# Optimization experiments

Hardware: AMD Instinct MI355X
Metric: run time of the kernel (lower is better)

The kernel has to match this reference:

```python
import jax, jax.numpy as jnp
import numpy as np

N, C, OUT, E, H = 4096, 256, 256, 131072, 8
DH = C // H
EPS = 1e-5


def layer_norm(h, g, b):
    mu = jnp.mean(h, axis=-1, keepdims=True)
    var = jnp.mean(jnp.square(h - mu), axis=-1, keepdims=True)
    return (h - mu) * jax.lax.rsqrt(var + EPS) * g + b


def setup_inputs() -> dict:
    key = jax.random.key(0)
    ks = jax.random.split(key, 12)
    s = 1.0 / np.sqrt(C)
    return {
        "x": jax.random.normal(ks[0], (N, C), jnp.float32),
        "edge_index": jax.random.randint(ks[1], (2, E), 0, N, jnp.int32),
        "edge_attr": jax.random.normal(ks[2], (E, C), jnp.float32),
        # nn.MultiheadAttention params
        "in_proj_w": jax.random.uniform(ks[3], (3 * C, C), jnp.float32, -s, s),
        "in_proj_b": jnp.zeros((3 * C,), jnp.float32),
        "attn_out_w": jax.random.uniform(ks[4], (C, C), jnp.float32, -s, s),
        "attn_out_b": jnp.zeros((C,), jnp.float32),
        # edge_mlp: Linear(3C -> OUT) + LayerNorm(OUT)
        "edge_w": jax.random.uniform(ks[5], (OUT, 3 * C), jnp.float32, -1 / np.sqrt(3 * C), 1 / np.sqrt(3 * C)),
        "edge_b": jax.random.uniform(ks[6], (OUT,), jnp.float32, -1 / np.sqrt(3 * C), 1 / np.sqrt(3 * C)),
        "ln1_g": jnp.ones((OUT,), jnp.float32),
        "ln1_b": jnp.zeros((OUT,), jnp.float32),
        # output_proj: Linear(C + OUT -> OUT)
        "out_w": jax.random.uniform(ks[7], (OUT, C + OUT), jnp.float32, -1 / np.sqrt(C + OUT), 1 / np.sqrt(C + OUT)),
        "out_b": jax.random.uniform(ks[8], (OUT,), jnp.float32, -1 / np.sqrt(C + OUT), 1 / np.sqrt(C + OUT)),
        "ln2_g": jnp.ones((OUT,), jnp.float32),
        "ln2_b": jnp.zeros((OUT,), jnp.float32),
    }


def reference(x, edge_index, edge_attr, in_proj_w, in_proj_b, attn_out_w, attn_out_b,
              edge_w, edge_b, ln1_g, ln1_b, out_w, out_b, ln2_g, ln2_b):
    num_nodes = x.shape[0]
    # --- dense self-attention over all nodes (seq len = N, batch 1) ---
    qkv = x @ in_proj_w.T + in_proj_b            # [N, 3C]
    q, k, v = jnp.split(qkv, 3, axis=-1)
    q = q.reshape(num_nodes, H, DH).transpose(1, 0, 2)  # [H, N, DH]
    k = k.reshape(num_nodes, H, DH).transpose(1, 0, 2)
    v = v.reshape(num_nodes, H, DH).transpose(1, 0, 2)
    scores = jnp.einsum("hqd,hkd->hqk", q, k) / np.sqrt(DH)
    attn = jax.nn.softmax(scores, axis=-1)       # dropout inactive at eval
    ctx = jnp.einsum("hqk,hkd->hqd", attn, v)    # [H, N, DH]
    ctx = ctx.transpose(1, 0, 2).reshape(num_nodes, C)
    x_attn = ctx @ attn_out_w.T + attn_out_b     # [N, C]
    # --- vectorized edge messages: gather -> MLP -> scatter-add ---
    row, col = edge_index[0], edge_index[1]
    msg_in = jnp.concatenate([x[row], x[col], edge_attr], axis=-1)  # [E, 3C]
    msg = jax.nn.relu(layer_norm(msg_in @ edge_w.T + edge_b, ln1_g, ln1_b))
    node_messages = jax.ops.segment_sum(msg, col, num_segments=num_nodes)  # [N, OUT]
    # --- combine, project, residual, norm ---
    combined = jnp.concatenate([x_attn, node_messages], axis=-1)
    out = combined @ out_w.T + out_b
    out = out + x                                # OUT == C so residual fires
    return layer_norm(out, ln2_g, ln2_b)
```

## Files before the change

### kernel.cpp

```cpp
#include <hip/hip_runtime.h>
#include <hip/hip_bf16.h>
#include <math.h>

typedef __bf16 bf16;
typedef __bf16 bf16x8 __attribute__((ext_vector_type(8)));
typedef __bf16 bf16x4 __attribute__((ext_vector_type(4)));
typedef float f32x4 __attribute__((ext_vector_type(4)));
typedef float f32x16 __attribute__((ext_vector_type(16)));

#define MFMA16(a, b, c) __builtin_amdgcn_mfma_f32_16x16x32_bf16((a), (b), (c), 0, 0, 0)
#define MFMA32(a, b, c) __builtin_amdgcn_mfma_f32_32x32x16_bf16((a), (b), (c), 0, 0, 0)

#define N_NODES 4096
#define C_DIM   256
#define E_EDGES 131072

__device__ __forceinline__ float ldf(const void* p, int i, bool f32) {
    return f32 ? ((const float*)p)[i] : (float)((const bf16*)p)[i];
}

__device__ __forceinline__ bf16x8 ld8(const void* base, size_t off, bool f32) {
    if (f32) {
        const float* p = (const float*)base + off;
        float4 a = *(const float4*)p;
        float4 b = *(const float4*)(p + 4);
        bf16x8 r;
        r[0] = (bf16)a.x; r[1] = (bf16)a.y; r[2] = (bf16)a.z; r[3] = (bf16)a.w;
        r[4] = (bf16)b.x; r[5] = (bf16)b.y; r[6] = (bf16)b.z; r[7] = (bf16)b.w;
        return r;
    }
    return *(const bf16x8*)((const bf16*)base + off);
}

__device__ __forceinline__ unsigned cvtpk(float a, float b) {
    unsigned r;
    asm("v_cvt_pk_bf16_f32 %0, %1, %2" : "=v"(r) : "v"(a), "v"(b));
    return r;
}
__device__ __forceinline__ void pl32swap(unsigned &a, unsigned &b) {
    asm volatile("v_permlane32_swap_b32 %0, %1" : "+v"(a), "+v"(b));
}

union PW { unsigned u[4]; bf16x8 v; };

__global__ __launch_bounds__(64) void detect_dtype(const void* x, int* flag)
{
    const bf16* xb = (const bf16*)x;
    int tid = threadIdx.x;
    int bad = 0;
    for (int i = tid; i < 4096; i += 64) {
        float v = fabsf((float)xb[i]);
        if (!(v >= 1e-6f && v <= 100.0f)) bad++;
    }
#pragma unroll
    for (int m = 1; m < 64; m <<= 1) bad += __shfl_xor(bad, m);
    if (tid == 0) *flag = (bad > 400) ? 1 : 0;
}

__global__ __launch_bounds__(256) void convert_inputs(
    const void* s0, const void* s1, const void* s2, const void* s3, const void* s4,
    bf16* dst, const int* flag)
{
    int idx = blockIdx.x * 256 + threadIdx.x;
    const void* src; int local;
    if (idx < 1048576)      { src = s0; local = idx; }
    else if (idx < 1245184) { src = s1; local = idx - 1048576; }
    else if (idx < 1310720) { src = s2; local = idx - 1245184; }
    else if (idx < 1507328) { src = s3; local = idx - 1310720; }
    else                    { src = s4; local = idx - 1507328; }
    if (*flag) dst[idx] = (bf16)(((const float*)src)[local]);
    else ((unsigned short*)dst)[idx] = ((const unsigned short*)src)[local];
}

__global__ __launch_bounds__(256) void edge_hist(
    const int* __restrict__ ecol, int* __restrict__ counts)
{
    int e = blockIdx.x * 256 + threadIdx.x;
    atomicAdd(&counts[ecol[e]], 1);
}

__global__ __launch_bounds__(256) void edge_scan(
    const int* __restrict__ counts, int* __restrict__ offsets,
    int* __restrict__ cursor)
{
    __shared__ int part[256];
    __shared__ int pref[257];
    int t = threadIdx.x;
    int base = t * 16;
    int s = 0;
#pragma unroll
    for (int i = 0; i < 16; ++i) s += counts[base + i];
    part[t] = s;
    __syncthreads();
    if (t == 0) {
        int run = 0;
        for (int i = 0; i < 256; ++i) { pref[i] = run; run += part[i]; }
        pref[256] = run;
    }
    __syncthreads();
    int off = pref[t];
#pragma unroll
    for (int i = 0; i < 16; ++i) {
        offsets[base + i] = off;
        cursor[base + i]  = off;
        off += counts[base + i];
    }
    if (t == 255) offsets[4096] = off;
}

__global__ __launch_bounds__(256) void edge_scatter(
    const int* __restrict__ ecol, int* __restrict__ cursor,
    int* __restrict__ eid)
{
    int e = blockIdx.x * 256 + threadIdx.x;
    int pos = atomicAdd(&cursor[ecol[e]], 1);
    eid[pos] = e;
}

__global__ __launch_bounds__(256) void gemm_bt(
    const bf16* __restrict__ A, int lda,
    const bf16* __restrict__ W, int ldw,
    const void* __restrict__ bias,
    void* __restrict__ Cout, int ldc, int c_f32,
    const bf16* __restrict__ resid, int ldr,
    int K, const int* __restrict__ flag)
{
    const bool f32 = (*flag != 0);
    const int wave = threadIdx.x >> 6;
    const int lane = threadIdx.x & 63;
    const int quad = lane >> 4;
    const int l16  = lane & 15;
    const int m_base = blockIdx.x * 32;
    const int n_base = blockIdx.y * 256 + wave * 64;

    const bf16* a0p = A + (size_t)(m_base + l16) * lda + quad * 8;
    const bf16* a1p = a0p + (size_t)16 * lda;
    const bf16* wp  = W + (size_t)(n_base + l16) * ldw + quad * 8;

    f32x4 acc[2][4] = {};
    for (int k = 0; k < K; k += 32) {
        bf16x8 a0 = *(const bf16x8*)(a0p + k);
        bf16x8 a1 = *(const bf16x8*)(a1p + k);
#pragma unroll
        for (int nt = 0; nt < 4; ++nt) {
            bf16x8 b = *(const bf16x8*)(wp + (size_t)nt * 16 * ldw + k);
            acc[0][nt] = MFMA16(a0, b, acc[0][nt]);
            acc[1][nt] = MFMA16(a1, b, acc[1][nt]);
        }
    }
#pragma unroll
    for (int mt = 0; mt < 2; ++mt) {
#pragma unroll
        for (int nt = 0; nt < 4; ++nt) {
            int col = n_base + nt * 16 + l16;
            float bv = bias ? ldf(bias, col, f32) : 0.0f;
#pragma unroll
            for (int r = 0; r < 4; ++r) {
                int row = m_base + mt * 16 + quad * 4 + r;
                float v = acc[mt][nt][r] + bv;
                if (resid) v += (float)resid[(size_t)row * ldr + col];
                if (c_f32) ((float*)Cout)[(size_t)row * ldc + col] = v;
                else       ((bf16*)Cout)[(size_t)row * ldc + col] = (bf16)v;
            }
        }
    }
}

__global__ __launch_bounds__(256) void gemm_uv(
    const bf16* __restrict__ x, const bf16* __restrict__ ew,
    bf16* __restrict__ U, bf16* __restrict__ V)
{
    const int wave = threadIdx.x >> 6;
    const int lane = threadIdx.x & 63;
    const int quad = lane >> 4;
    const int l16  = lane & 15;
    const int m_base = blockIdx.x * 32;
    bf16* dst = blockIdx.y ? V : U;
    const bf16* W = ew + blockIdx.y * 256;

    const bf16* a0p = x + (size_t)(m_base + l16) * 256 + quad * 8;
    const bf16* a1p = a0p + (size_t)16 * 256;
    const bf16* wp  = W + (size_t)(wave * 64 + l16) * 768 + quad * 8;

    f32x4 acc[2][4] = {};
#pragma unroll
    for (int kk = 0; kk < 8; ++kk) {
        int k = kk * 32;
        bf16x8 a0 = *(const bf16x8*)(a0p + k);
        bf16x8 a1 = *(const bf16x8*)(a1p + k);
#pragma unroll
        for (int nt = 0; nt < 4; ++nt) {
            bf16x8 b = *(const bf16x8*)(wp + (size_t)nt * 16 * 768 + k);
            acc[0][nt] = MFMA16(a0, b, acc[0][nt]);
            acc[1][nt] = MFMA16(a1, b, acc[1][nt]);
        }
    }
#pragma unroll
    for (int mt = 0; mt < 2; ++mt)
#pragma unroll
        for (int nt = 0; nt < 4; ++nt) {
            int col = wave * 64 + nt * 16 + l16;
#pragma unroll
            for (int r = 0; r < 4; ++r) {
                int row = m_base + mt * 16 + quad * 4 + r;
                dst[(size_t)row * 256 + col] = (bf16)acc[mt][nt][r];
            }
        }
}

__global__ __launch_bounds__(256) void transpose_v(
    const bf16* __restrict__ qkv, bf16* __restrict__ vt)
{
    __shared__ bf16 t[32][65];
    const int n0 = blockIdx.x * 64;
    const int c0 = blockIdx.y * 32;
    const int tid = threadIdx.x;
    {
        int cl = tid & 31, nl = tid >> 5;
#pragma unroll
        for (int p = 0; p < 8; ++p) {
            int n = nl + p * 8;
            t[cl][n] = qkv[(size_t)(n0 + n) * 768 + 512 + c0 + cl];
        }
    }
    __syncthreads();
    {
        int nn = tid & 63, cc = tid >> 6;
#pragma unroll
        for (int p = 0; p < 8; ++p) {
            int c = cc + p * 4;
            vt[(size_t)(c0 + c) * 4096 + n0 + nn] = t[c][nn];
        }
    }
}

__global__ __launch_bounds__(256) void attn_kernel(
    const bf16* __restrict__ qkv,
    const bf16* __restrict__ vt,
    bf16* __restrict__ ctx)
{
    __shared__ float oL[4][32][33];
    __shared__ float mS[4][32];
    __shared__ float lS[4][32];
    const int tid  = threadIdx.x;
    const int wave = tid >> 6;
    const int lane = tid & 63;
    const int l32  = lane & 31;
    const int hl   = lane >> 5;
    const int h  = blockIdx.x >> 7;
    const int qt = blockIdx.x & 127;

    const float csc = 1.4426950408889634f * 0.17677669529663687f;

    const bf16* qrow = qkv + (size_t)(qt * 32 + l32) * 768 + h * 32 + hl * 8;
    bf16x8 qf1 = *(const bf16x8*)qrow;
    bf16x8 qf2 = *(const bf16x8*)(qrow + 16);

    const bf16* kbp = qkv + 256 + h * 32 + hl * 8;
    const bf16* vrp = vt + (size_t)(h * 32 + l32) * 4096 + hl * 8;

    float mrun = -INFINITY, msc = -INFINITY, lacc = 0.f;
    f32x16 oacc = {};
    const f32x16 z16 = {};

    const int kbeg = wave * 1024;
    for (int k0 = kbeg; k0 < kbeg + 1024; k0 += 32) {
        const bf16* kp = kbp + (size_t)(k0 + l32) * 768;
        bf16x8 kf1 = *(const bf16x8*)kp;
        bf16x8 kf2 = *(const bf16x8*)(kp + 16);
        bf16x8 vf1 = *(const bf16x8*)(vrp + k0);
        bf16x8 vf2 = *(const bf16x8*)(vrp + k0 + 16);

        f32x16 s = MFMA32(kf1, qf1, z16);
        s = MFMA32(kf2, qf2, s);

        float a0 = fmaxf(fmaxf(s[0], s[1]), fmaxf(s[2], s[3]));
        float a1 = fmaxf(fmaxf(s[4], s[5]), fmaxf(s[6], s[7]));
        float a2 = fmaxf(fmaxf(s[8], s[9]), fmaxf(s[10], s[11]));
        float a3 = fmaxf(fmaxf(s[12], s[13]), fmaxf(s[14], s[15]));
        float tm = fmaxf(fmaxf(a0, a1), fmaxf(a2, a3));
        tm = fmaxf(tm, __shfl_xor(tm, 32));

        if (__any(tm > mrun)) {
            float nm = fmaxf(mrun, tm);
            float nmsc = nm * csc;
            float al = exp2f(msc - nmsc);
            mrun = nm; msc = nmsc;
            lacc *= al;
#pragma unroll
            for (int i = 0; i < 16; ++i) oacc[i] *= al;
        }

        float p[16];
#pragma unroll
        for (int i = 0; i < 16; ++i) {
            p[i] = exp2f(__builtin_fmaf(s[i], csc, -msc));
            lacc += p[i];
        }

        unsigned w0 = cvtpk(p[0], p[1]),  w1 = cvtpk(p[2], p[3]);
        unsigned w2 = cvtpk(p[4], p[5]),  w3 = cvtpk(p[6], p[7]);
        unsigned w4 = cvtpk(p[8], p[9]),  w5 = cvtpk(p[10], p[11]);
        unsigned w6 = cvtpk(p[12], p[13]), w7 = cvtpk(p[14], p[15]);
        pl32swap(w0, w2); pl32swap(w1, w3);
        pl32swap(w4, w6); pl32swap(w5, w7);
        PW f1; f1.u[0] = w0; f1.u[1] = w1; f1.u[2] = w2; f1.u[3] = w3;
        PW f2; f2.u[0] = w4; f2.u[1] = w5; f2.u[2] = w6; f2.u[3] = w7;

        oacc = MFMA32(vf1, f1.v, oacc);
        oacc = MFMA32(vf2, f2.v, oacc);
    }

    lacc += __shfl_xor(lacc, 32);
    if (hl == 0) { mS[wave][l32] = mrun; lS[wave][l32] = lacc; }
#pragma unroll
    for (int i = 0; i < 16; ++i) {
        int d = (i & 3) + 8 * (i >> 2) + 4 * hl;
        oL[wave][l32][d] = oacc[i];
    }
    __syncthreads();
    {
        int q = tid >> 3, d0 = (tid & 7) * 4;
        float m0 = mS[0][q], m1 = mS[1][q], m2 = mS[2][q], m3 = mS[3][q];
        float ms = fmaxf(fmaxf(m0, m1), fmaxf(m2, m3));
        float f0 = exp2f((m0 - ms) * csc), f1 = exp2f((m1 - ms) * csc);
        float f2 = exp2f((m2 - ms) * csc), f3 = exp2f((m3 - ms) * csc);
        float ls = lS[0][q] * f0 + lS[1][q] * f1 + lS[2][q] * f2 + lS[3][q] * f3;
        float inv = 1.0f / ls;
        bf16x4 o4;
#pragma unroll
        for (int i = 0; i < 4; ++i) {
            int d = d0 + i;
            float v = (oL[0][q][d] * f0 + oL[1][q][d] * f1 +
                       oL[2][q][d] * f2 + oL[3][q][d] * f3) * inv;
            o4[i] = (bf16)v;
        }
        *(bf16x4*)(ctx + (size_t)(qt * 32 + q) * 256 + h * 32 + d0) = o4;
    }
}

__global__ __launch_bounds__(256, 4) void edge_msg_v5(
    const int* __restrict__ erow, const int* __restrict__ ecol,
    const void* __restrict__ eattr,
    const bf16* __restrict__ ew,
    const void* __restrict__ eb,
    const void* __restrict__ g1, const void* __restrict__ b1,
    const bf16* __restrict__ U, const bf16* __restrict__ V,
    bf16* __restrict__ msg, const int* __restrict__ flag)
{
    __shared__ float stats[32][4][2];
    const bool f32 = (*flag != 0);
    const int tid  = threadIdx.x;
    const int colq = tid >> 6;
    const int lane = tid & 63;
    const int quad = lane >> 4;
    const int l16  = lane & 15;
    const int e_base = blockIdx.x * 32;

    const bf16* wp = ew + (size_t)(colq * 64 + l16) * 768 + 512 + quad * 8;

    f32x4 acc[2][4] = {};
#pragma unroll
    for (int k0 = 0; k0 < 8; ++k0) {
        bf16x8 b[4];
#pragma unroll
        for (int nt = 0; nt < 4; ++nt)
            b[nt] = *(const bf16x8*)(wp + (size_t)nt * 16 * 768 + k0 * 32);
#pragma unroll
        for (int mt = 0; mt < 2; ++mt) {
            bf16x8 a = ld8(eattr,
                (size_t)(e_base + mt * 16 + l16) * 256 + k0 * 32 + quad * 8, f32);
#pragma unroll
            for (int nt = 0; nt < 4; ++nt)
                acc[mt][nt] = MFMA16(a, b[nt], acc[mt][nt]);
        }
    }

    float ebv[4], glv[4], blv[4];
#pragma unroll
    for (int nt = 0; nt < 4; ++nt) {
        int col = colq * 64 + nt * 16 + l16;
        ebv[nt] = ldf(eb, col, f32);
        glv[nt] = ldf(g1, col, f32);
        blv[nt] = ldf(b1, col, f32);
    }
    int erw[2][4], ecl[2][4];
#pragma unroll
    for (int mt = 0; mt < 2; ++mt)
#pragma unroll
        for (int r = 0; r < 4; ++r) {
            int e = e_base + mt * 16 + quad * 4 + r;
            erw[mt][r] = erow[e];
            ecl[mt][r] = ecol[e];
        }

    float s[2][4] = {}, q[2][4] = {};
#pragma unroll
    for (int mt = 0; mt < 2; ++mt)
#pragma unroll
        for (int nt = 0; nt < 4; ++nt) {
            int col = colq * 64 + nt * 16 + l16;
#pragma unroll
            for (int r = 0; r < 4; ++r) {
                float u = (float)U[(size_t)erw[mt][r] * 256 + col];
                float v = (float)V[(size_t)ecl[mt][r] * 256 + col];
                float val = acc[mt][nt][r] + ebv[nt] + u + v;
                acc[mt][nt][r] = val;
                s[mt][r] += val;
                q[mt][r] = __builtin_fmaf(val, val, q[mt][r]);
            }
        }
#pragma unroll
    for (int msk = 1; msk < 16; msk <<= 1)
#pragma unroll
        for (int mt = 0; mt < 2; ++mt)
#pragma unroll
            for (int r = 0; r < 4; ++r) {
                s[mt][r] += __shfl_xor(s[mt][r], msk);
                q[mt][r] += __shfl_xor(q[mt][r], msk);
            }
    if (l16 == 0) {
#pragma unroll
        for (int mt = 0; mt < 2; ++mt)
#pragma unroll
            for (int r = 0; r < 4; ++r) {
                int row = mt * 16 + quad * 4 + r;
                stats[row][colq][0] = s[mt][r];
                stats[row][colq][1] = q[mt][r];
            }
    }
    __syncthreads();
#pragma unroll
    for (int mt = 0; mt < 2; ++mt)
#pragma unroll
        for (int r = 0; r < 4; ++r) {
            int row = mt * 16 + quad * 4 + r;
            float ss = (stats[row][0][0] + stats[row][1][0]) +
                       (stats[row][2][0] + stats[row][3][0]);
            float qq = (stats[row][0][1] + stats[row][1][1]) +
                       (stats[row][2][1] + stats[row][3][1]);
            float mean = ss * (1.0f / 256.0f);
            float var  = qq * (1.0f / 256.0f) - mean * mean;
            float rstd = rsqrtf(var + 1e-5f);
            bf16* op = msg + (size_t)(e_base + row) * 256;
#pragma unroll
            for (int nt = 0; nt < 4; ++nt) {
                int col = colq * 64 + nt * 16 + l16;
                float o = fmaxf((acc[mt][nt][r] - mean) * rstd * glv[nt] + blv[nt], 0.0f);
                op[col] = (bf16)o;
            }
        }
}

__global__ __launch_bounds__(256) void node_gather(
    const bf16* __restrict__ msg,
    const int* __restrict__ offsets, const int* __restrict__ eid,
    bf16* __restrict__ combined)
{
    const int wave = threadIdx.x >> 6, lane = threadIdx.x & 63;
    const int node = blockIdx.x * 4 + wave;
    const int start = offsets[node];
    const int cnt   = offsets[node + 1] - start;
    float a0 = 0.f, a1 = 0.f, a2 = 0.f, a3 = 0.f;
    int i = 0;
    for (; i + 4 <= cnt; i += 4) {
        int e0 = eid[start + i],     e1 = eid[start + i + 1];
        int e2 = eid[start + i + 2], e3 = eid[start + i + 3];
        bf16x4 r0 = *(const bf16x4*)(msg + (size_t)e0 * 256 + lane * 4);
        bf16x4 r1 = *(const bf16x4*)(msg + (size_t)e1 * 256 + lane * 4);
        bf16x4 r2 = *(const bf16x4*)(msg + (size_t)e2 * 256 + lane * 4);
        bf16x4 r3 = *(const bf16x4*)(msg + (size_t)e3 * 256 + lane * 4);
        a0 += (float)r0[0] + (float)r1[0] + (float)r2[0] + (float)r3[0];
        a1 += (float)r0[1] + (float)r1[1] + (float)r2[1] + (float)r3[1];
        a2 += (float)r0[2] + (float)r1[2] + (float)r2[2] + (float)r3[2];
        a3 += (float)r0[3] + (float)r1[3] + (float)r2[3] + (float)r3[3];
    }
    for (; i < cnt; ++i) {
        int e = eid[start + i];
        bf16x4 r = *(const bf16x4*)(msg + (size_t)e * 256 + lane * 4);
        a0 += (float)r[0]; a1 += (float)r[1]; a2 += (float)r[2]; a3 += (float)r[3];
    }
    bf16* cp = combined + (size_t)node * 512 + 256 + lane * 4;
    cp[0] = (bf16)a0; cp[1] = (bf16)a1; cp[2] = (bf16)a2; cp[3] = (bf16)a3;
}

__global__ __launch_bounds__(256) void edge_node(
    const bf16* __restrict__ x,
    const int* __restrict__ erow,
    const void* __restrict__ eattr,
    const bf16* __restrict__ ew,
    const void* __restrict__ eb,
    const void* __restrict__ g1, const void* __restrict__ b1,
    const int* __restrict__ offsets, const int* __restrict__ eid,
    bf16* __restrict__ combined, const int* __restrict__ flag)
{
    __shared__ float part[32][4][2];
    const bool f32 = (*flag != 0);
    const int wave = threadIdx.x >> 6;
    const int lane = threadIdx.x & 63;
    const int quad = lane >> 4;
    const int l16  = lane & 15;
    const int n = blockIdx.x;
    const int start = offsets[n];
    const int cnt   = offsets[n + 1] - start;

    float gv[4], bv[4], ebv[4];
#pragma unroll
    for (int nt = 0; nt < 4; ++nt) {
        int col = wave * 64 + nt * 16 + l16;
        gv[nt]  = ldf(g1, col, f32);
        bv[nt]  = ldf(b1, col, f32);
        ebv[nt] = ldf(eb, col, f32);
    }
    const bf16* wp = ew + (size_t)(wave * 64 + l16) * 768 + quad * 8;
    const bf16* xn = x + (size_t)n * 256 + quad * 8;

    f32x4 acc1[4] = {};
#pragma unroll
    for (int kk = 0; kk < 8; ++kk) {
        bf16x8 a = *(const bf16x8*)(xn + kk * 32);
#pragma unroll
        for (int nt = 0; nt < 4; ++nt) {
            bf16x8 b = *(const bf16x8*)(wp + (size_t)nt * 16 * 768 + 256 + kk * 32);
            acc1[nt] = MFMA16(a, b, acc1[nt]);
        }
    }
    float nacc[4] = {0.f, 0.f, 0.f, 0.f};
    for (int c0 = 0; c0 < cnt; c0 += 32) {
        int i0 = c0 + l16;      i0 = (i0 < cnt) ? i0 : 0;
        int i1 = c0 + 16 + l16; i1 = (i1 < cnt) ? i1 : 0;
        int e0 = eid[start + i0];
        int e1 = eid[start + i1];
        const bf16* xr0 = x + (size_t)erow[e0] * 256 + quad * 8;
        const bf16* xr1 = x + (size_t)erow[e1] * 256 + quad * 8;
        f32x4 acc[2][4];
#pragma unroll
        for (int nt = 0; nt < 4; ++nt) { acc[0][nt] = acc1[nt]; acc[1][nt] = acc1[nt]; }
#pragma unroll
        for (int kk = 0; kk < 8; ++kk) {
            bf16x8 a0 = *(const bf16x8*)(xr0 + kk * 32);
            bf16x8 a1 = *(const bf16x8*)(xr1 + kk * 32);
#pragma unroll
            for (int nt = 0; nt < 4; ++nt) {
                bf16x8 b = *(const bf16x8*)(wp + (size_t)nt * 16 * 768 + kk * 32);
                acc[0][nt] = MFMA16(a0, b, acc[0][nt]);
                acc[1][nt] = MFMA16(a1, b, acc[1][nt]);
            }
        }
#pragma unroll
        for (int kk = 0; kk < 8; ++kk) {
            int koff = quad * 8 + kk * 32;
            bf16x8 a0 = ld8(eattr, (size_t)e0 * 256 + koff, f32);
            bf16x8 a1 = ld8(eattr, (size_t)e1 * 256 + koff, f32);
#pragma unroll
            for (int nt = 0; nt < 4; ++nt) {
                bf16x8 b = *(const bf16x8*)(wp + (size_t)nt * 16 * 768 + 512 + kk * 32);
                acc[0][nt] = MFMA16(a0, b, acc[0][nt]);
                acc[1][nt] = MFMA16(a1, b, acc[1][nt]);
            }
        }
#pragma unroll
        for (int mt = 0; mt < 2; ++mt)
#pragma unroll
            for (int nt = 0; nt < 4; ++nt)
#pragma unroll
                for (int r = 0; r < 4; ++r) acc[mt][nt][r] += ebv[nt];
        float ps[2][4], pq[2][4];
#pragma unroll
        for (int mt = 0; mt < 2; ++mt)
#pragma unroll
            for (int r = 0; r < 4; ++r) {
                float s = 0.f, q = 0.f;
#pragma unroll
                for (int nt = 0; nt < 4; ++nt) {
                    float v = acc[mt][nt][r];
                    s += v; q += v * v;
                }
                ps[mt][r] = s; pq[mt][r] = q;
            }
#pragma unroll
        for (int msk = 1; msk < 16; msk <<= 1)
#pragma unroll
            for (int mt = 0; mt < 2; ++mt)
#pragma unroll
                for (int r = 0; r < 4; ++r) {
                    ps[mt][r] += __shfl_xor(ps[mt][r], msk);
                    pq[mt][r] += __shfl_xor(pq[mt][r], msk);
                }
        if (l16 == 0) {
#pragma unroll
            for (int mt = 0; mt < 2; ++mt)
#pragma unroll
                for (int r = 0; r < 4; ++r) {
                    part[mt * 16 + quad * 4 + r][wave][0] = ps[mt][r];
                    part[mt * 16 + quad * 4 + r][wave][1] = pq[mt][r];
                }
        }
        __syncthreads();
#pragma unroll
        for (int mt = 0; mt < 2; ++mt)
#pragma unroll
            for (int r = 0; r < 4; ++r) {
                int row = mt * 16 + quad * 4 + r;
                float s = part[row][0][0] + part[row][1][0] + part[row][2][0] + part[row][3][0];
                float q = part[row][0][1] + part[row][1][1] + part[row][2][1] + part[row][3][1];
                float mean = s * (1.0f / 256.0f);
                float var  = q * (1.0f / 256.0f) - mean * mean;
                float rstd = rsqrtf(var + 1e-5f);
                if ((c0 + row) < cnt) {
#pragma unroll
                    for (int nt = 0; nt < 4; ++nt) {
                        float val = (acc[mt][nt][r] - mean) * rstd * gv[nt] + bv[nt];
                        nacc[nt] += fmaxf(val, 0.0f);
                    }
                }
            }
        __syncthreads();
    }
#pragma unroll
    for (int nt = 0; nt < 4; ++nt) {
        nacc[nt] += __shfl_xor(nacc[nt], 16);
        nacc[nt] += __shfl_xor(nacc[nt], 32);
    }
    if (quad == 0) {
#pragma unroll
        for (int nt = 0; nt < 4; ++nt)
            combined[(size_t)n * 512 + 256 + wave * 64 + nt * 16 + l16] = (bf16)nacc[nt];
    }
}

__global__ __launch_bounds__(256) void gemm_ln(
    const bf16* __restrict__ A,
    const bf16* __restrict__ W,
    const void* __restrict__ bias,
    const bf16* __restrict__ resid,
    const void* __restrict__ g, const void* __restrict__ bb,
    void* __restrict__ out, const int* __restrict__ flag)
{
    __shared__ float stats[16][4][2];
    const bool f32 = (*flag != 0);
    const int wave = threadIdx.x >> 6;
    const int lane = threadIdx.x & 63;
    const int quad = lane >> 4;
    const int l16  = lane & 15;
    const int m_base = blockIdx.x * 16;

    const bf16* ap = A + (size_t)(m_base + l16) * 512 + quad * 8;
    const bf16* wp = W + (size_t)(wave * 64 + l16) * 512 + quad * 8;

    f32x4 acc[4] = {};
#pragma unroll
    for (int kk = 0; kk < 16; ++kk) {
        int k = kk * 32;
        bf16x8 a = *(const bf16x8*)(ap + k);
#pragma unroll
        for (int nt = 0; nt < 4; ++nt) {
            bf16x8 b = *(const bf16x8*)(wp + (size_t)nt * 16 * 512 + k);
            acc[nt] = MFMA16(a, b, acc[nt]);
        }
    }
    float s[4] = {}, q[4] = {};
#pragma unroll
    for (int nt = 0; nt < 4; ++nt) {
        int col = wave * 64 + nt * 16 + l16;
        float bv = ldf(bias, col, f32);
#pragma unroll
        for (int r = 0; r < 4; ++r) {
            int row = m_base + quad * 4 + r;
            float v = acc[nt][r] + bv + (float)resid[(size_t)row * 256 + col];
            acc[nt][r] = v;
            s[r] += v;
            q[r] = __builtin_fmaf(v, v, q[r]);
        }
    }
#pragma unroll
    for (int msk = 1; msk < 16; msk <<= 1)
#pragma unroll
        for (int r = 0; r < 4; ++r) {
            s[r] += __shfl_xor(s[r], msk);
            q[r] += __shfl_xor(q[r], msk);
        }
    if (l16 == 0) {
#pragma unroll
        for (int r = 0; r < 4; ++r) {
            stats[quad * 4 + r][wave][0] = s[r];
            stats[quad * 4 + r][wave][1] = q[r];
        }
    }
    __syncthreads();
#pragma unroll
    for (int r = 0; r < 4; ++r) {
        int row16 = quad * 4 + r;
        float ss = (stats[row16][0][0] + stats[row16][1][0]) +
                   (stats[row16][2][0] + stats[row16][3][0]);
        float qq = (stats[row16][0][1] + stats[row16][1][1]) +
                   (stats[row16][2][1] + stats[row16][3][1]);
        float mean = ss * (1.0f / 256.0f);
        float var  = qq * (1.0f / 256.0f) - mean * mean;
        float rstd = rsqrtf(var + 1e-5f);
        int row = m_base + row16;
#pragma unroll
        for (int nt = 0; nt < 4; ++nt) {
            int col = wave * 64 + nt * 16 + l16;
            float o = (acc[nt][r] - mean) * rstd * ldf(g, col, f32) + ldf(bb, col, f32);
            if (f32) ((float*)out)[(size_t)row * 256 + col] = o;
            else     ((bf16*)out)[(size_t)row * 256 + col] = (bf16)o;
        }
    }
}

extern "C" void kernel_launch(void* const* d_in, const int* in_sizes, int n_in,
                              void* d_out, int out_size, void* d_ws, size_t ws_size,
                              hipStream_t stream)
{
    const void* x_raw  = d_in[0];
    const int*  eidx   = (const int*)d_in[1];
    const void* eattr  = d_in[2];
    const void* in_w   = d_in[3];
    const void* in_b   = d_in[4];
    const void* ao_w   = d_in[5];
    const void* ao_b   = d_in[6];
    const void* e_w    = d_in[7];
    const void* e_b    = d_in[8];
    const void* g1     = d_in[9];
    const void* b1     = d_in[10];
    const void* o_w    = d_in[11];
    const void* o_b    = d_in[12];
    const void* g2     = d_in[13];
    const void* b2     = d_in[14];

    char* ws = (char*)d_ws;
    bf16*  qkv      = (bf16*)(ws);
    bf16*  vt       = (bf16*)(ws + 6291456);
    bf16*  ctx      = (bf16*)(ws + 8388608);
    bf16*  combined = (bf16*)(ws + 10485760);
    int*   counts   = (int*)(ws + 14680064);
    int*   offsets  = (int*)(ws + 14696448);
    int*   cursor   = (int*)(ws + 14712848);
    int*   eid      = (int*)(ws + 14729232);
    bf16*  U        = (bf16*)(ws + 18874368);
    bf16*  V        = (bf16*)(ws + 20971520);
    bf16*  canon    = (bf16*)(ws + 23068672);
    int*   flag     = (int*)(ws + 26345472);
    bf16*  msg      = (bf16*)(ws + 26345728);

    const size_t WS_NEEDED = 93454592;

    bf16* x_bf   = canon;
    bf16* inw_bf = canon + 1048576;
    bf16* aow_bf = canon + 1245184;
    bf16* ew_bf  = canon + 1310720;
    bf16* ow_bf  = canon + 1507328;

    const int* erow = eidx;
    const int* ecol = eidx + E_EDGES;

    detect_dtype<<<dim3(1), 64, 0, stream>>>(x_raw, flag);
    convert_inputs<<<dim3(6400), 256, 0, stream>>>(x_raw, in_w, ao_w, e_w, o_w,
                                                   canon, flag);
    hipMemsetAsync(counts, 0, 16384, stream);
    edge_hist<<<dim3(E_EDGES / 256), 256, 0, stream>>>(ecol, counts);
    edge_scan<<<dim3(1), 256, 0, stream>>>(counts, offsets, cursor);
    edge_scatter<<<dim3(E_EDGES / 256), 256, 0, stream>>>(ecol, cursor, eid);

    gemm_uv<<<dim3(128, 2), 256, 0, stream>>>(x_bf, ew_bf, U, V);

    gemm_bt<<<dim3(128, 3), 256, 0, stream>>>(x_bf, 256, inw_bf, 256, in_b,
                                              qkv, 768, 0, nullptr, 0, 256, flag);
    transpose_v<<<dim3(64, 8), 256, 0, stream>>>(qkv, vt);
    attn_kernel<<<dim3(1024), 256, 0, stream>>>(qkv, vt, ctx);
    gemm_bt<<<dim3(128, 1), 256, 0, stream>>>(ctx, 256, aow_bf, 256, ao_b,
                                              combined, 512, 0, nullptr, 0, 256, flag);
    if (ws_size >= WS_NEEDED) {
        edge_msg_v5<<<dim3(E_EDGES / 32), 256, 0, stream>>>(erow, ecol, eattr,
                                                            ew_bf, e_b, g1, b1,
                                                            U, V, msg, flag);
        node_gather<<<dim3(N_NODES / 4), 256, 0, stream>>>(msg, offsets, eid, combined);
    } else {
        edge_node<<<dim3(N_NODES), 256, 0, stream>>>(x_bf, erow, eattr,
                                                     ew_bf, e_b, g1, b1,
                                                     offsets, eid, combined, flag);
    }
    gemm_ln<<<dim3(256), 256, 0, stream>>>(combined, ow_bf, o_b, x_bf,
                                           g2, b2, d_out, flag);
}
```

Baseline: 517.4 us.

## Split edge MLP: GEMM writes pre-LN messages sorted by column, LN+sum per node

The edge kernel now only computes the edge_attr GEMM plus bias over 64-edge tiles, staging A in padded shared memory and holding weights in registers. It writes pre-LayerNorm rows, transposed through shared memory, directly into column-sorted positions using a new epos array from the scatter pass. A per-node kernel then reads contiguous pre-activations, adds the gathered U row and the node's V row, applies LayerNorm and ReLU per edge, and sums into combined. The aim is to replace the random U/V and message gathers with contiguous reads and drop the separate gather pass, at the cost of scattered row writes and wave-level LayerNorm reductions on the node side.

```diff
diff --git a/kernel.cpp b/kernel.cpp
--- a/kernel.cpp
+++ b/kernel.cpp
@@ -14,6 +14,8 @@
 #define N_NODES 4096
 #define C_DIM   256
 #define E_EDGES 131072
+#define APAD    280
+#define TPAD    260
 
 __device__ __forceinline__ float ldf(const void* p, int i, bool f32) {
     return f32 ? ((const float*)p)[i] : (float)((const bf16*)p)[i];
@@ -110,11 +112,12 @@
 
 __global__ __launch_bounds__(256) void edge_scatter(
     const int* __restrict__ ecol, int* __restrict__ cursor,
-    int* __restrict__ eid)
+    int* __restrict__ eid, int* __restrict__ epos)
 {
     int e = blockIdx.x * 256 + threadIdx.x;
     int pos = atomicAdd(&cursor[ecol[e]], 1);
     eid[pos] = e;
+    epos[e] = pos;
 }
 
 __global__ __launch_bounds__(256) void gemm_bt(
@@ -339,149 +342,173 @@
     }
 }
 
-__global__ __launch_bounds__(256, 4) void edge_msg_v5(
-    const int* __restrict__ erow, const int* __restrict__ ecol,
+__global__ __launch_bounds__(256) void edge_gemm(
     const void* __restrict__ eattr,
     const bf16* __restrict__ ew,
     const void* __restrict__ eb,
-    const void* __restrict__ g1, const void* __restrict__ b1,
-    const bf16* __restrict__ U, const bf16* __restrict__ V,
-    bf16* __restrict__ msg, const int* __restrict__ flag)
-{
-    __shared__ float stats[32][4][2];
+    const int* __restrict__ epos,
+    bf16* __restrict__ msgpre, const int* __restrict__ flag)
+{
+    __shared__ char smem[64 * APAD * 2];
+    bf16* Asm = (bf16*)smem;
+    float (*Trow)[TPAD] = (float(*)[TPAD])smem;
+
     const bool f32 = (*flag != 0);
     const int tid  = threadIdx.x;
-    const int colq = tid >> 6;
+    const int wave = tid >> 6;
     const int lane = tid & 63;
     const int quad = lane >> 4;
     const int l16  = lane & 15;
-    const int e_base = blockIdx.x * 32;
-
-    const bf16* wp = ew + (size_t)(colq * 64 + l16) * 768 + 512 + quad * 8;
-
-    f32x4 acc[2][4] = {};
+    const int e_base = blockIdx.x * 64;
+
+    bf16x8 breg[8][4];
+#pragma unroll
+    for (int k0 = 0; k0 < 8; ++k0)
+#pragma unroll
+        for (int nt = 0; nt < 4; ++nt)
+            breg[k0][nt] = *(const bf16x8*)(ew +
+                (size_t)(wave * 64 + nt * 16 + l16) * 768 + 512 + k0 * 32 + quad * 8);
+
+    {
+        int row   = tid >> 2;
+        int cbase = (tid & 3) * 64;
+        bf16* dst = Asm + row * APAD + cbase;
+        if (!f32) {
+            const bf16* src = (const bf16*)eattr + (size_t)(e_base + row) * 256 + cbase;
+#pragma unroll
+            for (int j = 0; j < 8; ++j)
+                *(bf16x8*)(dst + j * 8) = *(const bf16x8*)(src + j * 8);
+        } else {
+            const float* src = (const float*)eattr + (size_t)(e_base + row) * 256 + cbase;
+#pragma unroll
+            for (int j = 0; j < 8; ++j) {
+                float4 a = *(const float4*)(src + j * 8);
+                float4 b = *(const float4*)(src + j * 8 + 4);
+                bf16x8 r;
+                r[0] = (bf16)a.x; r[1] = (bf16)a.y; r[2] = (bf16)a.z; r[3] = (bf16)a.w;
+                r[4] = (bf16)b.x; r[5] = (bf16)b.y; r[6] = (bf16)b.z; r[7] = (bf16)b.w;
+                *(bf16x8*)(dst + j * 8) = r;
+            }
+        }
+    }
+    __syncthreads();
+
+    f32x4 acc[4][4] = {};
 #pragma unroll
     for (int k0 = 0; k0 < 8; ++k0) {
-        bf16x8 b[4];
-#pragma unroll
-        for (int nt = 0; nt < 4; ++nt)
-            b[nt] = *(const bf16x8*)(wp + (size_t)nt * 16 * 768 + k0 * 32);
-#pragma unroll
-        for (int mt = 0; mt < 2; ++mt) {
-            bf16x8 a = ld8(eattr,
-                (size_t)(e_base + mt * 16 + l16) * 256 + k0 * 32 + quad * 8, f32);
+#pragma unroll
+        for (int mt = 0; mt < 4; ++mt) {
+            bf16x8 af = *(const bf16x8*)(Asm + (mt * 16 + l16) * APAD + k0 * 32 + quad * 8);
 #pragma unroll
             for (int nt = 0; nt < 4; ++nt)
-                acc[mt][nt] = MFMA16(a, b[nt], acc[mt][nt]);
-        }
-    }
-
-    float ebv[4], glv[4], blv[4];
-#pragma unroll
-    for (int nt = 0; nt < 4; ++nt) {
-        int col = colq * 64 + nt * 16 + l16;
-        ebv[nt] = ldf(eb, col, f32);
-        glv[nt] = ldf(g1, col, f32);
-        blv[nt] = ldf(b1, col, f32);
-    }
-    int erw[2][4], ecl[2][4];
-#pragma unroll
-    for (int mt = 0; mt < 2; ++mt)
-#pragma unroll
-        for (int r = 0; r < 4; ++r) {
-            int e = e_base + mt * 16 + quad * 4 + r;
-            erw[mt][r] = erow[e];
-            ecl[mt][r] = ecol[e];
-        }
-
-    float s[2][4] = {}, q[2][4] = {};
-#pragma unroll
-    for (int mt = 0; mt < 2; ++mt)
-#pragma unroll
-        for (int nt = 0; nt < 4; ++nt) {
-            int col = colq * 64 + nt * 16 + l16;
-#pragma unroll
-            for (int r = 0; r < 4; ++r) {
-                float u = (float)U[(size_t)erw[mt][r] * 256 + col];
-                float v = (float)V[(size_t)ecl[mt][r] * 256 + col];
-                float val = acc[mt][nt][r] + ebv[nt] + u + v;
-                acc[mt][nt][r] = val;
-                s[mt][r] += val;
-                q[mt][r] = __builtin_fmaf(val, val, q[mt][r]);
+                acc[mt][nt] = MFMA16(af, breg[k0][nt], acc[mt][nt]);
+        }
+    }
+
+    float ebv[4];
+#pragma unroll
+    for (int nt = 0; nt < 4; ++nt)
+        ebv[nt] = ldf(eb, wave * 64 + nt * 16 + l16, f32);
+
+    for (int p = 0; p < 2; ++p) {
+        __syncthreads();
+#pragma unroll
+        for (int mtl = 0; mtl < 2; ++mtl) {
+            int mt = p * 2 + mtl;
+#pragma unroll
+            for (int nt = 0; nt < 4; ++nt)
+#pragma unroll
+                for (int r = 0; r < 4; ++r)
+                    Trow[mtl * 16 + quad * 4 + r][wave * 64 + nt * 16 + l16] =
+                        acc[mt][nt][r] + ebv[nt];
+        }
+        __syncthreads();
+        {
+            int row = tid >> 3;
+            int seg = tid & 7;
+            int ep = epos[e_base + p * 32 + row];
+            const float* tr = &Trow[row][seg * 32];
+            bf16* op = msgpre + (size_t)ep * 256 + seg * 32;
+#pragma unroll
+            for (int i = 0; i < 4; ++i) {
+                float4 a = *(const float4*)(tr + i * 8);
+                float4 b = *(const float4*)(tr + i * 8 + 4);
+                bf16x8 o;
+                o[0] = (bf16)a.x; o[1] = (bf16)a.y; o[2] = (bf16)a.z; o[3] = (bf16)a.w;
+                o[4] = (bf16)b.x; o[5] = (bf16)b.y; o[6] = (bf16)b.z; o[7] = (bf16)b.w;
+                *(bf16x8*)(op + i * 8) = o;
             }
         }
-#pragma unroll
-    for (int msk = 1; msk < 16; msk <<= 1)
-#pragma unroll
-        for (int mt = 0; mt < 2; ++mt)
-#pragma unroll
-            for (int r = 0; r < 4; ++r) {
-                s[mt][r] += __shfl_xor(s[mt][r], msk);
-                q[mt][r] += __shfl_xor(q[mt][r], msk);
-            }
-    if (l16 == 0) {
-#pragma unroll
-        for (int mt = 0; mt < 2; ++mt)
-#pragma unroll
-            for (int r = 0; r < 4; ++r) {
-                int row = mt * 16 + quad * 4 + r;
-                stats[row][colq][0] = s[mt][r];
-                stats[row][colq][1] = q[mt][r];
-            }
-    }
-    __syncthreads();
-#pragma unroll
-    for (int mt = 0; mt < 2; ++mt)
-#pragma unroll
-        for (int r = 0; r < 4; ++r) {
-            int row = mt * 16 + quad * 4 + r;
-            float ss = (stats[row][0][0] + stats[row][1][0]) +
-                       (stats[row][2][0] + stats[row][3][0]);
-            float qq = (stats[row][0][1] + stats[row][1][1]) +
-                       (stats[row][2][1] + stats[row][3][1]);
-            float mean = ss * (1.0f / 256.0f);
-            float var  = qq * (1.0f / 256.0f) - mean * mean;
-            float rstd = rsqrtf(var + 1e-5f);
-            bf16* op = msg + (size_t)(e_base + row) * 256;
-#pragma unroll
-            for (int nt = 0; nt < 4; ++nt) {
-                int col = colq * 64 + nt * 16 + l16;
-                float o = fmaxf((acc[mt][nt][r] - mean) * rstd * glv[nt] + blv[nt], 0.0f);
-                op[col] = (bf16)o;
-            }
-        }
-}
-
-__global__ __launch_bounds__(256) void node_gather(
-    const bf16* __restrict__ msg,
+    }
+}
+
+__global__ __launch_bounds__(256) void node_ln(
+    const bf16* __restrict__ msgpre,
     const int* __restrict__ offsets, const int* __restrict__ eid,
-    bf16* __restrict__ combined)
-{
-    const int wave = threadIdx.x >> 6, lane = threadIdx.x & 63;
-    const int node = blockIdx.x * 4 + wave;
+    const int* __restrict__ erow,
+    const bf16* __restrict__ U, const bf16* __restrict__ V,
+    const void* __restrict__ g1, const void* __restrict__ b1,
+    bf16* __restrict__ combined, const int* __restrict__ flag)
+{
+    __shared__ float accL[4][256];
+    const bool f32 = (*flag != 0);
+    const int wave = threadIdx.x >> 6;
+    const int lane = threadIdx.x & 63;
+    const int node = blockIdx.x;
     const int start = offsets[node];
     const int cnt   = offsets[node + 1] - start;
-    float a0 = 0.f, a1 = 0.f, a2 = 0.f, a3 = 0.f;
-    int i = 0;
-    for (; i + 4 <= cnt; i += 4) {
-        int e0 = eid[start + i],     e1 = eid[start + i + 1];
-        int e2 = eid[start + i + 2], e3 = eid[start + i + 3];
-        bf16x4 r0 = *(const bf16x4*)(msg + (size_t)e0 * 256 + lane * 4);
-        bf16x4 r1 = *(const bf16x4*)(msg + (size_t)e1 * 256 + lane * 4);
-        bf16x4 r2 = *(const bf16x4*)(msg + (size_t)e2 * 256 + lane * 4);
-        bf16x4 r3 = *(const bf16x4*)(msg + (size_t)e3 * 256 + lane * 4);
-        a0 += (float)r0[0] + (float)r1[0] + (float)r2[0] + (float)r3[0];
-        a1 += (float)r0[1] + (float)r1[1] + (float)r2[1] + (float)r3[1];
-        a2 += (float)r0[2] + (float)r1[2] + (float)r2[2] + (float)r3[2];
-        a3 += (float)r0[3] + (float)r1[3] + (float)r2[3] + (float)r3[3];
-    }
-    for (; i < cnt; ++i) {
-        int e = eid[start + i];
-        bf16x4 r = *(const bf16x4*)(msg + (size_t)e * 256 + lane * 4);
-        a0 += (float)r[0]; a1 += (float)r[1]; a2 += (float)r[2]; a3 += (float)r[3];
-    }
-    bf16* cp = combined + (size_t)node * 512 + 256 + lane * 4;
-    cp[0] = (bf16)a0; cp[1] = (bf16)a1; cp[2] = (bf16)a2; cp[3] = (bf16)a3;
+
+    float glv[4], blv[4], vv[4];
+#pragma unroll
+    for (int i = 0; i < 4; ++i) {
+        glv[i] = ldf(g1, lane * 4 + i, f32);
+        blv[i] = ldf(b1, lane * 4 + i, f32);
+    }
+    {
+        bf16x4 v4 = *(const bf16x4*)(V + (size_t)node * 256 + lane * 4);
+#pragma unroll
+        for (int i = 0; i < 4; ++i) vv[i] = (float)v4[i];
+    }
+
+    float nacc[4] = {0.f, 0.f, 0.f, 0.f};
+    for (int i = wave; i < cnt; i += 4) {
+        int pos = start + i;
+        int er = erow[eid[pos]];
+        bf16x4 t4 = *(const bf16x4*)(msgpre + (size_t)pos * 256 + lane * 4);
+        bf16x4 u4 = *(const bf16x4*)(U + (size_t)er * 256 + lane * 4);
+        float val[4];
+        float s = 0.f, q = 0.f;
+#pragma unroll
+        for (int j = 0; j < 4; ++j) {
+            val[j] = (float)t4[j] + (float)u4[j] + vv[j];
+            s += val[j];
+            q = __builtin_fmaf(val[j], val[j], q);
+        }
+#pragma unroll
+        for (int msk = 1; msk < 64; msk <<= 1) {
+            s += __shfl_xor(s, msk);
+            q += __shfl_xor(q, msk);
+        }
+        float mean = s * (1.0f / 256.0f);
+        float var  = q * (1.0f / 256.0f) - mean * mean;
+        float rstd = rsqrtf(var + 1e-5f);
+#pragma unroll
+        for (int j = 0; j < 4; ++j)
+            nacc[j] += fmaxf((val[j] - mean) * rstd * glv[j] + blv[j], 0.0f);
+    }
+#pragma unroll
+    for (int j = 0; j < 4; ++j) accL[wave][lane * 4 + j] = nacc[j];
+    __syncthreads();
+    if (wave == 0) {
+        bf16x4 o4;
+#pragma unroll
+        for (int j = 0; j < 4; ++j) {
+            int c = lane * 4 + j;
+            float s = (accL[0][c] + accL[1][c]) + (accL[2][c] + accL[3][c]);
+            o4[j] = (bf16)s;
+        }
+        *(bf16x4*)(combined + (size_t)node * 512 + 256 + lane * 4) = o4;
+    }
 }
 
 __global__ __launch_bounds__(256) void edge_node(
@@ -738,11 +765,12 @@
     int*   offsets  = (int*)(ws + 14696448);
     int*   cursor   = (int*)(ws + 14712848);
     int*   eid      = (int*)(ws + 14729232);
+    int*   epos     = (int*)(ws + 15253520);
     bf16*  U        = (bf16*)(ws + 18874368);
     bf16*  V        = (bf16*)(ws + 20971520);
     bf16*  canon    = (bf16*)(ws + 23068672);
     int*   flag     = (int*)(ws + 26345472);
-    bf16*  msg      = (bf16*)(ws + 26345728);
+    bf16*  msgpre   = (bf16*)(ws + 26345728);
 
     const size_t WS_NEEDED = 93454592;
 
@@ -761,7 +789,7 @@
     hipMemsetAsync(counts, 0, 16384, stream);
     edge_hist<<<dim3(E_EDGES / 256), 256, 0, stream>>>(ecol, counts);
     edge_scan<<<dim3(1), 256, 0, stream>>>(counts, offsets, cursor);
-    edge_scatter<<<dim3(E_EDGES / 256), 256, 0, stream>>>(ecol, cursor, eid);
+    edge_scatter<<<dim3(E_EDGES / 256), 256, 0, stream>>>(ecol, cursor, eid, epos);
 
     gemm_uv<<<dim3(128, 2), 256, 0, stream>>>(x_bf, ew_bf, U, V);
 
@@ -772,10 +800,10 @@
     gemm_bt<<<dim3(128, 1), 256, 0, stream>>>(ctx, 256, aow_bf, 256, ao_b,
                                               combined, 512, 0, nullptr, 0, 256, flag);
     if (ws_size >= WS_NEEDED) {
-        edge_msg_v5<<<dim3(E_EDGES / 32), 256, 0, stream>>>(erow, ecol, eattr,
-                                                            ew_bf, e_b, g1, b1,
-                                                            U, V, msg, flag);
-        node_gather<<<dim3(N_NODES / 4), 256, 0, stream>>>(msg, offsets, eid, combined);
+        edge_gemm<<<dim3(E_EDGES / 64), 256, 0, stream>>>(eattr, ew_bf, e_b,
+                                                          epos, msgpre, flag);
+        node_ln<<<dim3(N_NODES), 256, 0, stream>>>(msgpre, offsets, eid, erow,
+                                                   U, V, g1, b1, combined, flag);
     } else {
         edge_node<<<dim3(N_NODES), 256, 0, stream>>>(x_bf, erow, eattr,
                                                      ew_bf, e_b, g1, b1,
```

Result: faster. 466.4 us (-9.9%).
